# Kernel optimization log

Hardware: AMD Instinct MI355X
Metric: run time of the kernel (lower is better)

The kernel has to match this reference:

```python
import jax, jax.numpy as jnp
import numpy as np

B, S, D, H = 4, 1024, 1024, 16
DH = D // H
EPS = 1e-5


def setup_inputs() -> dict:
    key = jax.random.key(0)
    ks = jax.random.split(key, 8)
    return {
        "q": jax.random.normal(ks[0], (B, S, D), jnp.float32),
        "k": jax.random.normal(ks[1], (B, S, D), jnp.float32),
        "v": jax.random.normal(ks[2], (B, S, D), jnp.float32),
        "mask": jnp.ones((B, S), jnp.float32),
        "scores": jax.random.normal(ks[3], (B, H, S, S), jnp.float32),
        "W_proj": jax.random.normal(ks[4], (D, D), jnp.float32) / np.sqrt(D),
        "W_minus": jax.random.normal(ks[5], (D, 2 * D), jnp.float32) / np.sqrt(2 * D),
        "ln_w": jnp.ones((D,), jnp.float32),
        "ln_b": jnp.zeros((D,), jnp.float32),
        "c": jnp.zeros((1,), jnp.float32),
    }


def reference(q, k, v, mask, scores, W_proj, W_minus, ln_w, ln_b, c):
    # split heads: (B,S,D) -> (B,S,H,DH)
    qh = q.reshape(B, S, H, DH)
    kh = k.reshape(B, S, H, DH)
    vh = v.reshape(B, S, H, DH)
    # scaled QK^T plus learnable-scaled residual scores
    att_scores = jnp.einsum("bqhd,bkhd->bhqk", qh, kh) / np.sqrt(DH) + c[0] * scores
    # additive mask (mask is (B, kv_len))
    att_scores = att_scores - 1e8 * (1.0 - mask)[:, None, None, :]
    att = jax.nn.softmax(att_scores, axis=-1)
    ctx = jnp.einsum("bhqk,bkhd->bqhd", att, vh).reshape(B, S, D)
    # proj (bias-free linear); dropout is identity at inference
    x = ctx @ W_proj.T
    # concat -> minus linear -> LayerNorm
    cat = jnp.concatenate([q, x], axis=-1)
    y = cat @ W_minus.T
    mu = jnp.mean(y, axis=-1, keepdims=True)
    var = jnp.mean((y - mu) ** 2, axis=-1, keepdims=True)
    y = (y - mu) * jax.lax.rsqrt(var + EPS) * ln_w + ln_b
    return (y, att_scores)
```

## Files before the change

kernel.cpp:

```cpp
#include <hip/hip_runtime.h>
#include <hip/hip_bf16.h>
#include <math.h>

#define BB 4
#define SS 1024
#define DD 1024
#define HH 16
#define DHH 64
#define BHH (BB * HH)

#define LDB 88
#define LDC 68

typedef __attribute__((ext_vector_type(8))) short short8;
typedef __attribute__((ext_vector_type(4))) float f32x4;

__device__ __forceinline__ unsigned short f2bf(float x) {
  __hip_bfloat16 h = __float2bfloat16(x);
  return *reinterpret_cast<unsigned short*>(&h);
}

__device__ __forceinline__ void stageb(const unsigned short* __restrict__ src, int ld,
                                       unsigned short* __restrict__ dst, int tid) {
#pragma unroll
  for (int u = 0; u < 2; ++u) {
    int cidx = tid + 256 * u;
    int r = cidx >> 3;
    int c8 = (cidx & 7) * 8;
    float4 v = *reinterpret_cast<const float4*>(src + (size_t)r * ld + c8);
    *reinterpret_cast<float4*>(dst + r * LDB + c8) = v;
  }
}

__device__ __forceinline__ short8 ldfrag(const unsigned short* __restrict__ base,
                                         int row16, int kh, int lane) {
  const unsigned short* p = base + (size_t)(row16 + (lane & 15)) * LDB + kh + (lane >> 4) * 8;
  return *reinterpret_cast<const short8*>(p);
}

__device__ __forceinline__ void mfma_tile(const unsigned short* As, const unsigned short* Bs,
                                          int w, int lane, f32x4 acc[4]) {
#pragma unroll
  for (int kh = 0; kh < 64; kh += 32) {
    short8 b = ldfrag(Bs, w * 16, kh, lane);
#pragma unroll
    for (int mb = 0; mb < 4; ++mb) {
      short8 a = ldfrag(As, mb * 16, kh, lane);
      acc[mb] = __builtin_amdgcn_mfma_f32_16x16x32_bf16(a, b, acc[mb], 0, 0, 0);
    }
  }
}

__device__ __forceinline__ void acc_to_lds(float* Cs, const f32x4 acc[4], int w, int lane,
                                           float scale) {
  int quad = lane >> 4, col = w * 16 + (lane & 15);
#pragma unroll
  for (int mb = 0; mb < 4; ++mb)
#pragma unroll
    for (int r = 0; r < 4; ++r)
      Cs[(mb * 16 + quad * 4 + r) * LDC + col] = acc[mb][r] * scale;
}

__global__ __launch_bounds__(256) void cvt_kernel(const float* __restrict__ in,
                                                  unsigned short* __restrict__ out, int n4) {
  int i = blockIdx.x * 256 + threadIdx.x;
  if (i < n4) {
    float4 v = reinterpret_cast<const float4*>(in)[i];
    ushort4 o;
    o.x = f2bf(v.x); o.y = f2bf(v.y); o.z = f2bf(v.z); o.w = f2bf(v.w);
    reinterpret_cast<ushort4*>(out)[i] = o;
  }
}

__global__ __launch_bounds__(256) void vtrans_kernel(const float* __restrict__ v,
                                                     unsigned short* __restrict__ vT) {
  __shared__ unsigned short T[64 * LDC];
  int tid = threadIdx.x;
  int s0 = blockIdx.x * 64, bh = blockIdx.y;
  int b = bh >> 4, h = bh & 15;
#pragma unroll
  for (int u = 0; u < 4; ++u) {
    int f = tid + 256 * u;
    int r = f >> 4, c4 = (f & 15) * 4;
    float4 vv = *reinterpret_cast<const float4*>(v + ((size_t)(b * SS + s0 + r)) * DD + h * DHH + c4);
    T[(c4 + 0) * LDC + r] = f2bf(vv.x);
    T[(c4 + 1) * LDC + r] = f2bf(vv.y);
    T[(c4 + 2) * LDC + r] = f2bf(vv.z);
    T[(c4 + 3) * LDC + r] = f2bf(vv.w);
  }
  __syncthreads();
#pragma unroll
  for (int u = 0; u < 4; ++u) {
    int f = tid + 256 * u;
    int d = f >> 4, s4 = (f & 15) * 4;
    ushort4 o = *reinterpret_cast<const ushort4*>(&T[d * LDC + s4]);
    *reinterpret_cast<ushort4*>(vT + ((size_t)(bh * DHH + d)) * SS + s0 + s4) = o;
  }
}

__global__ __launch_bounds__(256) void attn_fused_kernel(
    const unsigned short* __restrict__ qb, const unsigned short* __restrict__ kb,
    const unsigned short* __restrict__ vT, const float* __restrict__ scores,
    const float* __restrict__ mask, const float* __restrict__ c,
    float* __restrict__ att, unsigned short* __restrict__ ctxb) {
  __shared__ unsigned short Ps[64 * LDB];
  __shared__ unsigned short Ks[64 * LDB];
  __shared__ unsigned short Vs[64 * LDB];
  __shared__ float Cs[64 * LDC];
  __shared__ float mrun[64], lrun[64], ascale[64];
  int tid = threadIdx.x, lane = tid & 63, w = tid >> 6;
  int qt = blockIdx.x, bh = blockIdx.y;
  int b = bh >> 4, h = bh & 15;
  int qr0 = qt * 64;

  stageb(qb + ((size_t)(b * SS + qr0)) * DD + h * DHH, DD, Ps, tid);
  if (tid < 64) { mrun[tid] = -3.0e38f; lrun[tid] = 0.0f; }
  __syncthreads();

  short8 qa[2][4];
#pragma unroll
  for (int kh = 0; kh < 2; ++kh)
#pragma unroll
    for (int mb = 0; mb < 4; ++mb)
      qa[kh][mb] = ldfrag(Ps, mb * 16, kh * 32, lane);

  float cc = c[0];
  f32x4 accO[4] = {};

  for (int kt = 0; kt < 16; ++kt) {
    int kr0 = kt * 64;
    stageb(kb + ((size_t)(b * SS + kr0)) * DD + h * DHH, DD, Ks, tid);
    stageb(vT + (size_t)bh * DHH * SS + kr0, SS, Vs, tid);
    __syncthreads();

    f32x4 acc[4] = {};
#pragma unroll
    for (int kh = 0; kh < 2; ++kh) {
      short8 bfr = ldfrag(Ks, w * 16, kh * 32, lane);
#pragma unroll
      for (int mb = 0; mb < 4; ++mb)
        acc[mb] = __builtin_amdgcn_mfma_f32_16x16x32_bf16(qa[kh][mb], bfr, acc[mb], 0, 0, 0);
    }
    acc_to_lds(Cs, acc, w, lane, 0.125f);
    __syncthreads();

#pragma unroll
    for (int u = 0; u < 4; ++u) {
      int f = tid + 256 * u;
      int row = f >> 4, c4 = (f & 15) * 4;
      int rg = bh * SS + qr0 + row;
      size_t goff = (size_t)rg * SS + kr0 + c4;
      float4 qk = *reinterpret_cast<const float4*>(&Cs[row * LDC + c4]);
      float4 sc = *reinterpret_cast<const float4*>(scores + goff);
      float4 mv = *reinterpret_cast<const float4*>(mask + b * SS + kr0 + c4);
      float o0 = qk.x + cc * sc.x - 1e8f * (1.0f - mv.x);
      float o1 = qk.y + cc * sc.y - 1e8f * (1.0f - mv.y);
      float o2 = qk.z + cc * sc.z - 1e8f * (1.0f - mv.z);
      float o3 = qk.w + cc * sc.w - 1e8f * (1.0f - mv.w);
      float4 ov = {o0, o1, o2, o3};
      *reinterpret_cast<float4*>(att + goff) = ov;
      float m = fmaxf(fmaxf(o0, o1), fmaxf(o2, o3));
#pragma unroll
      for (int off = 1; off <= 8; off <<= 1) m = fmaxf(m, __shfl_xor(m, off));
      float mo = mrun[row];
      float mn = fmaxf(mo, m);
      float e0 = __expf(o0 - mn), e1 = __expf(o1 - mn);
      float e2 = __expf(o2 - mn), e3 = __expf(o3 - mn);
      float l = e0 + e1 + e2 + e3;
#pragma unroll
      for (int off = 1; off <= 8; off <<= 1) l += __shfl_xor(l, off);
      ushort4 pv;
      pv.x = f2bf(e0); pv.y = f2bf(e1); pv.z = f2bf(e2); pv.w = f2bf(e3);
      *reinterpret_cast<ushort4*>(&Ps[row * LDB + c4]) = pv;
      if ((tid & 15) == 0) {
        float a = __expf(mo - mn);
        lrun[row] = lrun[row] * a + l;
        mrun[row] = mn;
        ascale[row] = a;
      }
    }
    __syncthreads();

#pragma unroll
    for (int mb = 0; mb < 4; ++mb) {
      int rb = mb * 16 + (lane >> 4) * 4;
      accO[mb][0] *= ascale[rb + 0];
      accO[mb][1] *= ascale[rb + 1];
      accO[mb][2] *= ascale[rb + 2];
      accO[mb][3] *= ascale[rb + 3];
    }
    mfma_tile(Ps, Vs, w, lane, accO);
    __syncthreads();
  }

#pragma unroll
  for (int mb = 0; mb < 4; ++mb) {
    int rb = mb * 16 + (lane >> 4) * 4;
    accO[mb][0] *= 1.0f / lrun[rb + 0];
    accO[mb][1] *= 1.0f / lrun[rb + 1];
    accO[mb][2] *= 1.0f / lrun[rb + 2];
    accO[mb][3] *= 1.0f / lrun[rb + 3];
  }
  acc_to_lds(Cs, accO, w, lane, 1.0f);
  __syncthreads();
#pragma unroll
  for (int u = 0; u < 4; ++u) {
    int f = tid + 256 * u;
    int row = f >> 4, c4 = (f & 15) * 4;
    float4 vv = *reinterpret_cast<const float4*>(&Cs[row * LDC + c4]);
    ushort4 o;
    o.x = f2bf(vv.x); o.y = f2bf(vv.y); o.z = f2bf(vv.z); o.w = f2bf(vv.w);
    *reinterpret_cast<ushort4*>(ctxb + ((size_t)(b * SS + qr0 + row)) * DD + h * DHH + c4) = o;
  }
}

__global__ __launch_bounds__(256) void proj_mfma_kernel(
    const unsigned short* __restrict__ A, const unsigned short* __restrict__ W,
    unsigned short* __restrict__ X) {
  __shared__ unsigned short smem[2 * 64 * LDB];
  unsigned short* As = smem;
  unsigned short* Bs = smem + 64 * LDB;
  float* Cs = reinterpret_cast<float*>(smem);
  int tid = threadIdx.x, lane = tid & 63, w = tid >> 6;
  int d0 = blockIdx.x * 64, n0 = blockIdx.y * 64;
  f32x4 acc[4] = {};
  for (int kc = 0; kc < DD; kc += 64) {
    stageb(A + (size_t)n0 * DD + kc, DD, As, tid);
    stageb(W + (size_t)d0 * DD + kc, DD, Bs, tid);
    __syncthreads();
    mfma_tile(As, Bs, w, lane, acc);
    __syncthreads();
  }
  acc_to_lds(Cs, acc, w, lane, 1.0f);
  __syncthreads();
#pragma unroll
  for (int u = 0; u < 4; ++u) {
    int f = tid + 256 * u;
    int row = f >> 4, c4 = (f & 15) * 4;
    float4 vv = *reinterpret_cast<const float4*>(&Cs[row * LDC + c4]);
    ushort4 o;
    o.x = f2bf(vv.x); o.y = f2bf(vv.y); o.z = f2bf(vv.z); o.w = f2bf(vv.w);
    *reinterpret_cast<ushort4*>(X + (size_t)(n0 + row) * DD + d0 + c4) = o;
  }
}

__global__ __launch_bounds__(256) void minus_mfma_kernel(
    const unsigned short* __restrict__ qb, const unsigned short* __restrict__ xb,
    const unsigned short* __restrict__ Wm, float* __restrict__ Y) {
  __shared__ unsigned short smem[2 * 64 * LDB];
  unsigned short* As = smem;
  unsigned short* Bs = smem + 64 * LDB;
  float* Cs = reinterpret_cast<float*>(smem);
  int tid = threadIdx.x, lane = tid & 63, w = tid >> 6;
  int d0 = blockIdx.x * 64, n0 = blockIdx.y * 64;
  f32x4 acc[4] = {};
  for (int kc = 0; kc < 2 * DD; kc += 64) {
    const unsigned short* asrc = (kc < DD) ? (qb + (size_t)n0 * DD + kc)
                                           : (xb + (size_t)n0 * DD + (kc - DD));
    stageb(asrc, DD, As, tid);
    stageb(Wm + (size_t)d0 * (2 * DD) + kc, 2 * DD, Bs, tid);
    __syncthreads();
    mfma_tile(As, Bs, w, lane, acc);
    __syncthreads();
  }
  acc_to_lds(Cs, acc, w, lane, 1.0f);
  __syncthreads();
#pragma unroll
  for (int u = 0; u < 4; ++u) {
    int f = tid + 256 * u;
    int row = f >> 4, c4 = (f & 15) * 4;
    float4 vv = *reinterpret_cast<const float4*>(&Cs[row * LDC + c4]);
    *reinterpret_cast<float4*>(Y + (size_t)(n0 + row) * DD + d0 + c4) = vv;
  }
}

__global__ __launch_bounds__(256) void ln_kernel(
    float* __restrict__ Y, const float* __restrict__ w, const float* __restrict__ b) {
  __shared__ float ps[4], ps2[4];
  int row = blockIdx.x, t = threadIdx.x;
  float* rp = Y + (size_t)row * DD;
  float4 v = *reinterpret_cast<const float4*>(rp + t * 4);
  float s = v.x + v.y + v.z + v.w;
  float s2 = v.x * v.x + v.y * v.y + v.z * v.z + v.w * v.w;
#pragma unroll
  for (int o = 32; o > 0; o >>= 1) {
    s += __shfl_down(s, o);
    s2 += __shfl_down(s2, o);
  }
  if ((t & 63) == 0) { ps[t >> 6] = s; ps2[t >> 6] = s2; }
  __syncthreads();
  s = ps[0] + ps[1] + ps[2] + ps[3];
  s2 = ps2[0] + ps2[1] + ps2[2] + ps2[3];
  float mu = s * (1.0f / DD);
  float var = s2 * (1.0f / DD) - mu * mu;
  float rs = rsqrtf(var + 1e-5f);
  float4 wv = *reinterpret_cast<const float4*>(w + t * 4);
  float4 bv = *reinterpret_cast<const float4*>(b + t * 4);
  float4 ov;
  ov.x = (v.x - mu) * rs * wv.x + bv.x;
  ov.y = (v.y - mu) * rs * wv.y + bv.y;
  ov.z = (v.z - mu) * rs * wv.z + bv.z;
  ov.w = (v.w - mu) * rs * wv.w + bv.w;
  *reinterpret_cast<float4*>(rp + t * 4) = ov;
}

extern "C" void kernel_launch(void* const* d_in, const int* in_sizes, int n_in,
                              void* d_out, int out_size, void* d_ws, size_t ws_size,
                              hipStream_t stream) {
  const float* q      = (const float*)d_in[0];
  const float* k      = (const float*)d_in[1];
  const float* v      = (const float*)d_in[2];
  const float* mask   = (const float*)d_in[3];
  const float* scores = (const float*)d_in[4];
  const float* W_proj = (const float*)d_in[5];
  const float* W_minus= (const float*)d_in[6];
  const float* ln_w   = (const float*)d_in[7];
  const float* ln_b   = (const float*)d_in[8];
  const float* c      = (const float*)d_in[9];

  float* y   = (float*)d_out;
  float* att = y + (size_t)BB * SS * DD;

  const size_t MB = 1u << 20;
  char* w = (char*)d_ws;
  unsigned short* qb   = (unsigned short*)(w);
  unsigned short* kb   = (unsigned short*)(w + 8 * MB);
  unsigned short* vT   = (unsigned short*)(w + 16 * MB);
  unsigned short* Wpb  = (unsigned short*)(w + 24 * MB);
  unsigned short* Wmb  = (unsigned short*)(w + 26 * MB);
  unsigned short* ctxb = (unsigned short*)(w + 30 * MB);
  unsigned short* xb   = (unsigned short*)(w + 38 * MB);

  const int NQ = BB * SS * DD;
  cvt_kernel<<<dim3(NQ / 4 / 256), 256, 0, stream>>>(q, qb, NQ / 4);
  cvt_kernel<<<dim3(NQ / 4 / 256), 256, 0, stream>>>(k, kb, NQ / 4);
  cvt_kernel<<<dim3(DD * DD / 4 / 256), 256, 0, stream>>>(W_proj, Wpb, DD * DD / 4);
  cvt_kernel<<<dim3(2 * DD * DD / 4 / 256), 256, 0, stream>>>(W_minus, Wmb, 2 * DD * DD / 4);
  vtrans_kernel<<<dim3(16, BHH), 256, 0, stream>>>(v, vT);

  attn_fused_kernel<<<dim3(16, BHH), 256, 0, stream>>>(qb, kb, vT, scores, mask, c, att, ctxb);
  proj_mfma_kernel<<<dim3(16, 64), 256, 0, stream>>>(ctxb, Wpb, xb);
  minus_mfma_kernel<<<dim3(16, 64), 256, 0, stream>>>(qb, xb, Wmb, y);
  ln_kernel<<<dim3(BB * SS), 256, 0, stream>>>(y, ln_w, ln_b);
}
```

Measured before the change: 761.1 us.

## Prefetch next K/V tiles and scores into registers, remap block order

The attention kernel now loads the next K/V tile and the next scores/mask chunk into registers while the current tile is computed, then writes them to LDS after the PV MFMA. This hides global-load latency behind compute. It also remaps the block index so that consecutive blocks cover different (b,h) pairs, which changes L2 locality for K/V. The MFMA sections are raised with s_setprio. The cost is higher register pressure, which can lower occupancy, plus an extra barrier per iteration.

```diff
diff --git a/kernel.cpp b/kernel.cpp
--- a/kernel.cpp
+++ b/kernel.cpp
@@ -109,12 +109,46 @@
   __shared__ float Cs[64 * LDC];
   __shared__ float mrun[64], lrun[64], ascale[64];
   int tid = threadIdx.x, lane = tid & 63, w = tid >> 6;
-  int qt = blockIdx.x, bh = blockIdx.y;
+
+  int flat = blockIdx.x + 16 * blockIdx.y;
+  int bh = (flat & 7) * 8 + ((flat >> 3) & 7);
+  int qt = flat >> 6;
   int b = bh >> 4, h = bh & 15;
   int qr0 = qt * 64;
 
+  int r0 = tid >> 3, c80 = (tid & 7) * 8;
+  int r1 = r0 + 32;
+  const unsigned short* kB = kb + (size_t)b * SS * DD + h * DHH;
+  const unsigned short* vB = vT + (size_t)bh * DHH * SS;
+  unsigned short* KsW0 = Ks + r0 * LDB + c80;
+  unsigned short* KsW1 = Ks + r1 * LDB + c80;
+  unsigned short* VsW0 = Vs + r0 * LDB + c80;
+  unsigned short* VsW1 = Vs + r1 * LDB + c80;
+
+  int rowe = tid >> 4;
+  int c4 = (tid & 15) * 4;
+  size_t eOff = ((size_t)(bh * SS + qr0 + rowe)) * SS + c4;
+  size_t mkOff = (size_t)b * SS + c4;
+
   stageb(qb + ((size_t)(b * SS + qr0)) * DD + h * DHH, DD, Ps, tid);
+  {
+    float4 k0 = *reinterpret_cast<const float4*>(kB + (size_t)r0 * DD + c80);
+    float4 k1 = *reinterpret_cast<const float4*>(kB + (size_t)r1 * DD + c80);
+    float4 v0 = *reinterpret_cast<const float4*>(vB + (size_t)r0 * SS + c80);
+    float4 v1 = *reinterpret_cast<const float4*>(vB + (size_t)r1 * SS + c80);
+    *reinterpret_cast<float4*>(KsW0) = k0;
+    *reinterpret_cast<float4*>(KsW1) = k1;
+    *reinterpret_cast<float4*>(VsW0) = v0;
+    *reinterpret_cast<float4*>(VsW1) = v1;
+  }
   if (tid < 64) { mrun[tid] = -3.0e38f; lrun[tid] = 0.0f; }
+
+  float4 sc[4];
+#pragma unroll
+  for (int u2 = 0; u2 < 4; ++u2)
+    sc[u2] = *reinterpret_cast<const float4*>(scores + eOff + (size_t)u2 * 16 * SS);
+  float4 mk = *reinterpret_cast<const float4*>(mask + mkOff);
+
   __syncthreads();
 
   short8 qa[2][4];
@@ -129,11 +163,17 @@
 
   for (int kt = 0; kt < 16; ++kt) {
     int kr0 = kt * 64;
-    stageb(kb + ((size_t)(b * SS + kr0)) * DD + h * DHH, DD, Ks, tid);
-    stageb(vT + (size_t)bh * DHH * SS + kr0, SS, Vs, tid);
-    __syncthreads();
+    float4 kn0 = {}, kn1 = {}, vn0 = {}, vn1 = {};
+    if (kt < 15) {
+      int kr = kr0 + 64;
+      kn0 = *reinterpret_cast<const float4*>(kB + (size_t)(kr + r0) * DD + c80);
+      kn1 = *reinterpret_cast<const float4*>(kB + (size_t)(kr + r1) * DD + c80);
+      vn0 = *reinterpret_cast<const float4*>(vB + (size_t)r0 * SS + kr + c80);
+      vn1 = *reinterpret_cast<const float4*>(vB + (size_t)r1 * SS + kr + c80);
+    }
 
     f32x4 acc[4] = {};
+    __builtin_amdgcn_s_setprio(1);
 #pragma unroll
     for (int kh = 0; kh < 2; ++kh) {
       short8 bfr = ldfrag(Ks, w * 16, kh * 32, lane);
@@ -141,24 +181,20 @@
       for (int mb = 0; mb < 4; ++mb)
         acc[mb] = __builtin_amdgcn_mfma_f32_16x16x32_bf16(qa[kh][mb], bfr, acc[mb], 0, 0, 0);
     }
+    __builtin_amdgcn_s_setprio(0);
     acc_to_lds(Cs, acc, w, lane, 0.125f);
     __syncthreads();
 
 #pragma unroll
-    for (int u = 0; u < 4; ++u) {
-      int f = tid + 256 * u;
-      int row = f >> 4, c4 = (f & 15) * 4;
-      int rg = bh * SS + qr0 + row;
-      size_t goff = (size_t)rg * SS + kr0 + c4;
+    for (int u2 = 0; u2 < 4; ++u2) {
+      int row = rowe + 16 * u2;
       float4 qk = *reinterpret_cast<const float4*>(&Cs[row * LDC + c4]);
-      float4 sc = *reinterpret_cast<const float4*>(scores + goff);
-      float4 mv = *reinterpret_cast<const float4*>(mask + b * SS + kr0 + c4);
-      float o0 = qk.x + cc * sc.x - 1e8f * (1.0f - mv.x);
-      float o1 = qk.y + cc * sc.y - 1e8f * (1.0f - mv.y);
-      float o2 = qk.z + cc * sc.z - 1e8f * (1.0f - mv.z);
-      float o3 = qk.w + cc * sc.w - 1e8f * (1.0f - mv.w);
+      float o0 = qk.x + cc * sc[u2].x - 1e8f * (1.0f - mk.x);
+      float o1 = qk.y + cc * sc[u2].y - 1e8f * (1.0f - mk.y);
+      float o2 = qk.z + cc * sc[u2].z - 1e8f * (1.0f - mk.z);
+      float o3 = qk.w + cc * sc[u2].w - 1e8f * (1.0f - mk.w);
       float4 ov = {o0, o1, o2, o3};
-      *reinterpret_cast<float4*>(att + goff) = ov;
+      *reinterpret_cast<float4*>(att + eOff + (size_t)u2 * 16 * SS + kr0) = ov;
       float m = fmaxf(fmaxf(o0, o1), fmaxf(o2, o3));
 #pragma unroll
       for (int off = 1; off <= 8; off <<= 1) m = fmaxf(m, __shfl_xor(m, off));
@@ -179,6 +215,12 @@
         ascale[row] = a;
       }
     }
+    if (kt < 15) {
+#pragma unroll
+      for (int u2 = 0; u2 < 4; ++u2)
+        sc[u2] = *reinterpret_cast<const float4*>(scores + eOff + (size_t)u2 * 16 * SS + kr0 + 64);
+      mk = *reinterpret_cast<const float4*>(mask + mkOff + kr0 + 64);
+    }
     __syncthreads();
 
 #pragma unroll
@@ -189,8 +231,17 @@
       accO[mb][2] *= ascale[rb + 2];
       accO[mb][3] *= ascale[rb + 3];
     }
+    __builtin_amdgcn_s_setprio(1);
     mfma_tile(Ps, Vs, w, lane, accO);
-    __syncthreads();
+    __builtin_amdgcn_s_setprio(0);
+    __syncthreads();
+    if (kt < 15) {
+      *reinterpret_cast<float4*>(KsW0) = kn0;
+      *reinterpret_cast<float4*>(KsW1) = kn1;
+      *reinterpret_cast<float4*>(VsW0) = vn0;
+      *reinterpret_cast<float4*>(VsW1) = vn1;
+      __syncthreads();
+    }
   }
 
 #pragma unroll
@@ -206,11 +257,11 @@
 #pragma unroll
   for (int u = 0; u < 4; ++u) {
     int f = tid + 256 * u;
-    int row = f >> 4, c4 = (f & 15) * 4;
-    float4 vv = *reinterpret_cast<const float4*>(&Cs[row * LDC + c4]);
+    int row = f >> 4, cc4 = (f & 15) * 4;
+    float4 vv = *reinterpret_cast<const float4*>(&Cs[row * LDC + cc4]);
     ushort4 o;
     o.x = f2bf(vv.x); o.y = f2bf(vv.y); o.z = f2bf(vv.z); o.w = f2bf(vv.w);
-    *reinterpret_cast<ushort4*>(ctxb + ((size_t)(b * SS + qr0 + row)) * DD + h * DHH + c4) = o;
+    *reinterpret_cast<ushort4*>(ctxb + ((size_t)(b * SS + qr0 + row)) * DD + h * DHH + cc4) = o;
   }
 }
 
```

After: 676.2 us. 1.13x faster.
